# Optimization experiments

Measured on AMD Instinct MI355X. Metric: run time of the kernel, lower is better.

## Reference

```python
import jax, jax.numpy as jnp
import numpy as np

N = 768          # number of proposals (graph nodes)
C = 1024         # box_head feature dim (in_feats)
HC = 256         # RelPN hidden_c
K = 20           # topk edges per node
GH = 256         # gcn_hidden
H1 = 4           # gat1 heads
IMG_H, IMG_W = 800.0, 800.0
NEG_SLOPE = 0.2  # PyG GATConv leaky_relu slope


def setup_inputs() -> dict:
    key = jax.random.key(0)
    ks = jax.random.split(key, 24)
    s = 0.02
    feats = jax.random.normal(ks[0], (N, C), jnp.float32)
    # valid boxes inside an 800x800 image
    cx = jax.random.uniform(ks[1], (N,), minval=100.0, maxval=700.0)
    cy = jax.random.uniform(ks[2], (N,), minval=100.0, maxval=700.0)
    w = jax.random.uniform(ks[3], (N,), minval=10.0, maxval=200.0)
    h = jax.random.uniform(ks[4], (N,), minval=10.0, maxval=200.0)
    boxes = jnp.stack([cx - 0.5 * w, cy - 0.5 * h, cx + 0.5 * w, cy + 0.5 * h], axis=1)
    rn = lambda k, sh: jax.random.normal(k, sh, jnp.float32) * s
    return {
        'feats': feats, 'boxes': boxes,
        # RelationProposalNetwork: fc1(2C+4 -> HC), fc2(HC -> 1)
        'W1': rn(ks[5], (2 * C + 4, HC)), 'b1': jnp.zeros((HC,), jnp.float32),
        'W2': rn(ks[6], (HC, 1)), 'b2': jnp.zeros((1,), jnp.float32),
        # GATConv(C+4 -> GH, heads=4)
        'g1W': rn(ks[7], (C + 4, H1 * GH)), 'g1as': rn(ks[8], (H1, GH)),
        'g1ad': rn(ks[9], (H1, GH)), 'g1b': jnp.zeros((H1 * GH,), jnp.float32),
        # GATConv(GH*4 -> 2, heads=1)
        'g2W': rn(ks[10], (H1 * GH, 2)), 'g2as': rn(ks[11], (1, 2)),
        'g2ad': rn(ks[12], (1, 2)), 'g2b': jnp.zeros((2,), jnp.float32),
        'rW1': rn(ks[13], (H1 * GH + 4, GH // 2)), 'rb1': jnp.zeros((GH // 2,), jnp.float32),
        'rW2': rn(ks[14], (GH // 2, 4)), 'rb2': jnp.zeros((4,), jnp.float32),
    }


def _gat(xin, W, a_src, a_dst, bias, heads, feat, nbr):
    """PyG-style GATConv (eval mode, self-loops already in nbr). nbr: [N, K+1] src ids per dst."""
    n = xin.shape[0]
    xp = (xin @ W).reshape(n, heads, feat)              # [N,H,F]
    asrc = jnp.einsum('nhf,hf->nh', xp, a_src)          # [N,H]
    adst = jnp.einsum('nhf,hf->nh', xp, a_dst)          # [N,H]
    logits = jax.nn.leaky_relu(asrc[nbr] + adst[:, None, :], NEG_SLOPE)  # [N,K+1,H]
    alpha = jax.nn.softmax(logits, axis=1)              # softmax over incoming edges per dst
    out = jnp.einsum('nkh,nkhf->nhf', alpha, xp[nbr])   # gather + weighted aggregate
    return out.reshape(n, heads * feat) + bias


def reference(feats, boxes, W1, b1, W2, b2, g1W, g1as, g1ad, g1b,
              g2W, g2as, g2ad, g2b, rW1, rb1, rW2, rb2):
    n = feats.shape[0]
    scale = jnp.array([IMG_W, IMG_H, IMG_W, IMG_H], jnp.float32)
    geom = boxes / scale                                 # _box_geom: normalized coords
    x = jnp.concatenate([feats, geom], axis=1)           # [N, C+4]

    # --- RelationProposalNetwork: fc1(cat[f_i, f_j, |b_i - b_j|]) decomposed ---
    Wa, Wb, Wg = W1[:C], W1[C:2 * C], W1[2 * C:]
    fa = feats @ Wa                                      # i-part  [N,HC]
    fb = feats @ Wb                                      # j-part  [N,HC]
    gdiff = jnp.abs(boxes[:, None, :] - boxes[None, :, :])          # [N,N,4]
    h = jax.nn.relu(fa[:, None, :] + fb[None, :, :]
                    + jnp.einsum('ijd,dh->ijh', gdiff, Wg) + b1)    # [N,N,HC]
    rel = jnp.einsum('ijh,h->ij', h, W2[:, 0]) + b2[0]              # [N,N]

    # --- top-k edges per destination node (exclude self), plus self-loops ---
    rel_masked = jnp.where(jnp.eye(n, dtype=bool), -1e9, rel)
    _, nbr = jax.lax.top_k(rel_masked, K)                # [N,K] src j for each dst i
    nbr = jnp.concatenate([nbr, jnp.arange(n)[:, None]], axis=1)    # [N,K+1]

    # --- GAT propagation ---
    h1 = jax.nn.relu(_gat(x, g1W, g1as, g1ad, g1b, H1, GH, nbr))    # [N,1024]
    logits = _gat(h1, g2W, g2as, g2ad, g2b, 1, 2, nbr)              # [N,2]

    reg_in = jnp.concatenate([h1, geom], axis=1)
    delta = jax.nn.relu(reg_in @ rW1 + rb1) @ rW2 + rb2             # [N,4]
    px0, py0, px1, py1 = boxes[:, 0], boxes[:, 1], boxes[:, 2], boxes[:, 3]
    pw, ph = px1 - px0, py1 - py0
    pcx, pcy = px0 + 0.5 * pw, py0 + 0.5 * ph
    dx, dy, dw, dh = delta[:, 0], delta[:, 1], delta[:, 2], delta[:, 3]
    gcx, gcy = dx * pw + pcx, dy * ph + pcy
    gw, gh = jnp.exp(dw) * pw, jnp.exp(dh) * ph
    final_boxes = jnp.stack([gcx - 0.5 * gw, gcy - 0.5 * gh,
                             gcx + 0.5 * gw, gcy + 0.5 * gh], axis=1)
    return jnp.concatenate([logits, final_boxes], axis=1)  # [N,6]
```

## Files before the change

### kernel.cpp

```cpp
#include <hip/hip_runtime.h>
#include <math.h>

#define NN 768
#define KK_TOP 20
#define NBR_K 21

typedef __attribute__((ext_vector_type(8))) short bf16x8;
typedef __attribute__((ext_vector_type(4))) float f32x4;
typedef unsigned short ushort_t;
typedef unsigned int uint_t;

__device__ __forceinline__ ushort_t f2bf(float x) {
    union { float f; uint_t u; } c; c.f = x;
    uint_t r = (c.u + 0x7FFFu + ((c.u >> 16) & 1u)) >> 16;
    return (ushort_t)r;
}
__device__ __forceinline__ float bf2f(ushort_t u) {
    union { uint_t u; float f; } c; c.u = ((uint_t)u) << 16;
    return c.f;
}

struct Params {
    const float *feats, *boxes, *W1, *b1, *W2, *b2;
    const float *g1W, *g1as, *g1ad, *g1b, *g2W, *g2as, *g2ad, *g2b;
    const float *rW1, *rb1, *rW2, *rb2;
    float *out;
    float *fafb, *xp, *relm, *hid, *Arow, *Brow, *asrc, *adst, *xp2, *aux2;
    float4 *wgt4; float *w2p, *consts;
    float *va, *vb, *av;
    int *nbr;
    ushort_t *featsbf, *btAB, *btG, *btR, *h1bf;
};

__global__ __launch_bounds__(256) void k_prep(Params P)
{
    int b = blockIdx.x, t = threadIdx.x;
    if (b == 800) {
        const float* Wg = P.W1 + 2048 * 256;
        float q0 = Wg[t], q1 = Wg[256 + t], q2 = Wg[512 + t], q3 = Wg[768 + t];
        float w2 = P.W2[t];
        P.wgt4[t] = make_float4(q0, q1, q2, q3);
        P.w2p[t] = w2;
        __shared__ float red[256];
        float vals[5] = {q0 * w2, q1 * w2, q2 * w2, q3 * w2, P.b1[t] * w2};
        for (int d = 0; d < 5; d++) {
            red[t] = vals[d]; __syncthreads();
            for (int s = 128; s > 0; s >>= 1) {
                if (t < s) red[t] += red[t + s];
                __syncthreads();
            }
            if (t == 0) P.consts[d] = red[0];
            __syncthreads();
        }
        return;
    }
    if (b >= 1313) {
        int o = (b - 1313) * 4 + (t >> 6);
        int lane = t & 63;
        if (o >= 8224) return;
        int vec = o / 1028, k = o - vec * 1028;
        int h = vec & 3;
        const float4* aw = (const float4*)(((vec < 4) ? P.g1as : P.g1ad) + h * 256);
        const float4* gw = (const float4*)(P.g1W + (size_t)k * 1024 + h * 256);
        float4 a = aw[lane], g = gw[lane];
        float s = a.x * g.x + a.y * g.y + a.z * g.z + a.w * g.w;
#pragma unroll
        for (int off = 32; off > 0; off >>= 1) s += __shfl_xor(s, off);
        if (lane == 0) P.av[o] = s;
        return;
    }
    if (b >= 801) {
        int o = (b - 801) * 4 + (t >> 6);
        int lane = t & 63;
        const float4* row = (const float4*)(P.W1 + (size_t)o * 256);
        float4 w = ((const float4*)P.W2)[lane];
        float4 f = row[lane];
        float s = f.x * w.x + f.y * w.y + f.z * w.z + f.w * w.w;
#pragma unroll
        for (int off = 32; off > 0; off >>= 1) s += __shfl_xor(s, off);
        if (lane == 0) { if (o < 1024) P.va[o] = s; else P.vb[o - 1024] = s; }
        return;
    }
    if (b >= 416) {
        int gid = (b - 416) * 2048 + t * 8;
        float4 v0 = *(const float4*)(P.feats + gid);
        float4 v1 = *(const float4*)(P.feats + gid + 4);
        uint4 r;
        r.x = (uint_t)f2bf(v0.x) | ((uint_t)f2bf(v0.y) << 16);
        r.y = (uint_t)f2bf(v0.z) | ((uint_t)f2bf(v0.w) << 16);
        r.z = (uint_t)f2bf(v1.x) | ((uint_t)f2bf(v1.y) << 16);
        r.w = (uint_t)f2bf(v1.z) | ((uint_t)f2bf(v1.w) << 16);
        *(uint4*)(P.featsbf + gid) = r;
        return;
    }
    const float* in; ushort_t* out; int ldN, tk, tn;
    if (b < 64)       { in = P.W1;              out = P.btAB;              ldN = 256;  tn = b & 3;  tk = b >> 2; }
    else if (b < 128) { int i = b - 64;  in = P.W1 + 1024 * 256; out = P.btAB + 256 * 1024; ldN = 256;  tn = i & 3;  tk = i >> 2; }
    else if (b < 384) { int i = b - 128; in = P.g1W;             out = P.btG;               ldN = 1024; tn = i & 15; tk = i >> 4; }
    else              { int i = b - 384; in = P.rW1;             out = P.btR;               ldN = 128;  tn = i & 1;  tk = i >> 1; }

    __shared__ __align__(16) float tile[64][68];
    int k0 = tk * 64, n0 = tn * 64;
#pragma unroll
    for (int it = 0; it < 4; it++) {
        int r = (t >> 4) + it * 16;
        int c = (t & 15) * 4;
        *(float4*)&tile[r][c] = *(const float4*)(in + (size_t)(k0 + r) * ldN + n0 + c);
    }
    __syncthreads();
    int n = t >> 2;
    int kc = (t & 3) * 16;
    uint_t p[8];
#pragma unroll
    for (int h = 0; h < 8; h++) {
        ushort_t lo = f2bf(tile[kc + 2 * h][n]);
        ushort_t hi = f2bf(tile[kc + 2 * h + 1][n]);
        p[h] = (uint_t)lo | ((uint_t)hi << 16);
    }
    ushort_t* dst = out + (size_t)(n0 + n) * 1024 + k0 + kc;
    *(uint4*)dst = make_uint4(p[0], p[1], p[2], p[3]);
    *(uint4*)(dst + 8) = make_uint4(p[4], p[5], p[6], p[7]);
}

__device__ __forceinline__ void mfma_unit(
    int bx, int by, const ushort_t* __restrict__ A, const ushort_t* __restrict__ Bt,
    float* __restrict__ C, int ldc, int mode,
    const float* __restrict__ boxes, const float* __restrict__ Wgeo,
    const float* __restrict__ bias, int t, char* smem)
{
    ushort_t (*As)[72] = (ushort_t(*)[72])smem;
    ushort_t (*Bs)[72] = (ushort_t(*)[72])(smem + 64 * 72 * 2);
    int m0 = by * 64, n0 = bx * 64;
    int lane = t & 63, w = t >> 6;
    int quad = lane >> 4, ci = lane & 15;

    int r0 = t >> 3, q0 = t & 7;
    int r1 = (t + 256) >> 3, q1 = (t + 256) & 7;

    const ushort_t* Abase = A + (size_t)(m0 + r0) * 1024 + q0 * 8;
    const ushort_t* Abase1 = A + (size_t)(m0 + r1) * 1024 + q1 * 8;
    const ushort_t* Bbase = Bt + (size_t)(n0 + r0) * 1024 + q0 * 8;
    const ushort_t* Bbase1 = Bt + (size_t)(n0 + r1) * 1024 + q1 * 8;

    uint4 pa0 = *(const uint4*)(Abase);
    uint4 pa1 = *(const uint4*)(Abase1);
    uint4 pb0 = *(const uint4*)(Bbase);
    uint4 pb1 = *(const uint4*)(Bbase1);

    f32x4 acc[2][2];
    acc[0][0] = (f32x4){0.f, 0.f, 0.f, 0.f};
    acc[0][1] = (f32x4){0.f, 0.f, 0.f, 0.f};
    acc[1][0] = (f32x4){0.f, 0.f, 0.f, 0.f};
    acc[1][1] = (f32x4){0.f, 0.f, 0.f, 0.f};

    int arow = (w & 1) * 32 + ci;
    int brow = (w >> 1) * 32 + ci;

    for (int kt = 0; kt < 16; kt++) {
        *(uint4*)&As[r0][q0 * 8] = pa0;
        *(uint4*)&As[r1][q1 * 8] = pa1;
        *(uint4*)&Bs[r0][q0 * 8] = pb0;
        *(uint4*)&Bs[r1][q1 * 8] = pb1;
        __syncthreads();
        if (kt < 15) {
            int ko = (kt + 1) * 64;
            pa0 = *(const uint4*)(Abase + ko);
            pa1 = *(const uint4*)(Abase1 + ko);
            pb0 = *(const uint4*)(Bbase + ko);
            pb1 = *(const uint4*)(Bbase1 + ko);
        }
#pragma unroll
        for (int s = 0; s < 2; s++) {
            int kb = s * 32 + quad * 8;
            bf16x8 a0 = *(const bf16x8*)&As[arow][kb];
            bf16x8 a1 = *(const bf16x8*)&As[arow + 16][kb];
            bf16x8 b0 = *(const bf16x8*)&Bs[brow][kb];
            bf16x8 b1 = *(const bf16x8*)&Bs[brow + 16][kb];
            acc[0][0] = __builtin_amdgcn_mfma_f32_16x16x32_bf16(a0, b0, acc[0][0], 0, 0, 0);
            acc[0][1] = __builtin_amdgcn_mfma_f32_16x16x32_bf16(a0, b1, acc[0][1], 0, 0, 0);
            acc[1][0] = __builtin_amdgcn_mfma_f32_16x16x32_bf16(a1, b0, acc[1][0], 0, 0, 0);
            acc[1][1] = __builtin_amdgcn_mfma_f32_16x16x32_bf16(a1, b1, acc[1][1], 0, 0, 0);
        }
        __syncthreads();
    }

    const float inv800 = 1.0f / 800.0f;
#pragma unroll
    for (int ni = 0; ni < 2; ni++) {
        int col = n0 + (w >> 1) * 32 + ni * 16 + ci;
        float wg0 = 0.f, wg1 = 0.f, wg2 = 0.f, wg3 = 0.f, bv = 0.f;
        if (mode) {
            wg0 = Wgeo[col]; wg1 = Wgeo[ldc + col];
            wg2 = Wgeo[2 * ldc + col]; wg3 = Wgeo[3 * ldc + col];
            if (mode == 2) bv = bias[col];
        }
#pragma unroll
        for (int mi = 0; mi < 2; mi++) {
            int rbase = m0 + (w & 1) * 32 + mi * 16 + quad * 4;
#pragma unroll
            for (int reg = 0; reg < 4; reg++) {
                int row = rbase + reg;
                float v = acc[mi][ni][reg];
                if (mode) {
                    float4 bx4 = *(const float4*)(boxes + row * 4);
                    v += (bx4.x * wg0 + bx4.y * wg1 + bx4.z * wg2 + bx4.w * wg3) * inv800 + bv;
                    if (mode == 2) v = fmaxf(v, 0.f);
                }
                C[(size_t)row * ldc + col] = v;
            }
        }
    }
}

__global__ __launch_bounds__(256) void k_gemms(Params P)
{
    __shared__ __align__(16) char smem[18432];
    int u = blockIdx.x, t = threadIdx.x;
    if (u < 96) {
        mfma_unit(u & 7, u >> 3, P.featsbf, P.btAB, P.fafb, 512, 0,
                  nullptr, nullptr, nullptr, t, smem);
    } else if (u < 288) {
        int v = u - 96;
        mfma_unit(v & 15, v >> 4, P.featsbf, P.btG, P.xp, 1024, 1,
                  P.boxes, P.g1W + (size_t)1024 * 1024, nullptr, t, smem);
    } else if (u < 480) {
        int row = (u - 288) * 4 + (t >> 6);
        int lane = t & 63;
        const float4* fr = (const float4*)(P.feats + (size_t)row * 1024);
        const float4* va4 = (const float4*)P.va;
        const float4* vb4 = (const float4*)P.vb;
        float s1 = 0.f, s2 = 0.f;
#pragma unroll
        for (int it = 0; it < 4; it++) {
            int idx = it * 64 + lane;
            float4 f = fr[idx], a = va4[idx], b = vb4[idx];
            s1 += f.x * a.x + f.y * a.y + f.z * a.z + f.w * a.w;
            s2 += f.x * b.x + f.y * b.y + f.z * b.z + f.w * b.w;
        }
#pragma unroll
        for (int off = 32; off > 0; off >>= 1) {
            s1 += __shfl_xor(s1, off);
            s2 += __shfl_xor(s2, off);
        }
        if (lane == 0) { P.Arow[row] = s1; P.Brow[row] = s2; }
    } else {
        int pair = (u - 480) * 4 + (t >> 6);
        int lane = t & 63;
        int n = pair >> 2, h = pair & 3;
        const float4* fr = (const float4*)(P.feats + (size_t)n * 1024);
        const float* vs = P.av + h * 1028;
        const float* vd = P.av + (4 + h) * 1028;
        const float4* vs4 = (const float4*)vs;
        const float4* vd4 = (const float4*)vd;
        float s1 = 0.f, s2 = 0.f;
#pragma unroll
        for (int it = 0; it < 4; it++) {
            int idx = it * 64 + lane;
            float4 f = fr[idx], a = vs4[idx], b = vd4[idx];
            s1 += f.x * a.x + f.y * a.y + f.z * a.z + f.w * a.w;
            s2 += f.x * b.x + f.y * b.y + f.z * b.z + f.w * b.w;
        }
#pragma unroll
        for (int off = 32; off > 0; off >>= 1) {
            s1 += __shfl_xor(s1, off);
            s2 += __shfl_xor(s2, off);
        }
        if (lane == 0) {
            const float inv800 = 1.0f / 800.0f;
            float4 bx = *(const float4*)(P.boxes + n * 4);
            float g0 = bx.x * inv800, g1 = bx.y * inv800, g2 = bx.z * inv800, g3 = bx.w * inv800;
            s1 += g0 * vs[1024] + g1 * vs[1025] + g2 * vs[1026] + g3 * vs[1027];
            s2 += g0 * vd[1024] + g1 * vd[1025] + g2 * vd[1026] + g3 * vd[1027];
            P.asrc[n * 4 + h] = s1;
            P.adst[n * 4 + h] = s2;
        }
    }
}

#define REL_ACC(FA0, FA1, FB0, FB1, Q, W)                                           \
    {                                                                               \
        float v;                                                                    \
        v = FA0 + FB0;                                                              \
        v = fmaf(g00.x, Q.x, v); v = fmaf(g00.y, Q.y, v);                           \
        v = fmaf(g00.z, Q.z, v); v = fmaf(g00.w, Q.w, v);                           \
        acc00 = fmaf(fabsf(v), W, acc00);                                           \
        v = FA0 + FB1;                                                              \
        v = fmaf(g01.x, Q.x, v); v = fmaf(g01.y, Q.y, v);                           \
        v = fmaf(g01.z, Q.z, v); v = fmaf(g01.w, Q.w, v);                           \
        acc01 = fmaf(fabsf(v), W, acc01);                                           \
        v = FA1 + FB0;                                                              \
        v = fmaf(g10.x, Q.x, v); v = fmaf(g10.y, Q.y, v);                           \
        v = fmaf(g10.z, Q.z, v); v = fmaf(g10.w, Q.w, v);                           \
        acc10 = fmaf(fabsf(v), W, acc10);                                           \
        v = FA1 + FB1;                                                              \
        v = fmaf(g11.x, Q.x, v); v = fmaf(g11.y, Q.y, v);                           \
        v = fmaf(g11.z, Q.z, v); v = fmaf(g11.w, Q.w, v);                           \
        acc11 = fmaf(fabsf(v), W, acc11);                                           \
    }

__global__ __launch_bounds__(256) void k_rel(Params P)
{
    __shared__ __align__(16) float fas[32][68];
    __shared__ __align__(16) float fbs[32][68];
    int t = threadIdx.x;
    int bx = blockIdx.x % 24, by = blockIdx.x / 24;
    int tx = t & 15, ty = t >> 4;
    int i0 = by * 32, j0 = bx * 32;
    int ia = i0 + ty, ib = i0 + ty + 16;
    int ja = j0 + tx, jb = j0 + tx + 16;

    float4 Bi0 = *(const float4*)(P.boxes + ia * 4);
    float4 Bi1 = *(const float4*)(P.boxes + ib * 4);
    float4 Bj0 = *(const float4*)(P.boxes + ja * 4);
    float4 Bj1 = *(const float4*)(P.boxes + jb * 4);
    float4 g00 = make_float4(fabsf(Bi0.x - Bj0.x), fabsf(Bi0.y - Bj0.y), fabsf(Bi0.z - Bj0.z), fabsf(Bi0.w - Bj0.w));
    float4 g01 = make_float4(fabsf(Bi0.x - Bj1.x), fabsf(Bi0.y - Bj1.y), fabsf(Bi0.z - Bj1.z), fabsf(Bi0.w - Bj1.w));
    float4 g10 = make_float4(fabsf(Bi1.x - Bj0.x), fabsf(Bi1.y - Bj0.y), fabsf(Bi1.z - Bj0.z), fabsf(Bi1.w - Bj0.w));
    float4 g11 = make_float4(fabsf(Bi1.x - Bj1.x), fabsf(Bi1.y - Bj1.y), fabsf(Bi1.z - Bj1.z), fabsf(Bi1.w - Bj1.w));

    float acc00 = 0.f, acc01 = 0.f, acc10 = 0.f, acc11 = 0.f;

    for (int p = 0; p < 4; p++) {
        for (int e = t; e < 512; e += 256) {
            int r = e >> 4, cq = e & 15;
            float4 bb = *(const float4*)(P.b1 + p * 64 + cq * 4);
            float4 fv = *(const float4*)(P.fafb + (size_t)(i0 + r) * 512 + p * 64 + cq * 4);
            float4 gv = *(const float4*)(P.fafb + (size_t)(j0 + r) * 512 + 256 + p * 64 + cq * 4);
            *(float4*)&fas[r][cq * 4] = make_float4(fv.x + bb.x, fv.y + bb.y, fv.z + bb.z, fv.w + bb.w);
            *(float4*)&fbs[r][cq * 4] = gv;
        }
        __syncthreads();
        const float4* wg = P.wgt4 + p * 64;
        const float* w2 = P.w2p + p * 64;
#pragma unroll 8
        for (int hc = 0; hc < 16; hc++) {
            int h4 = hc * 4;
            float4 fa0 = *(const float4*)&fas[ty][h4];
            float4 fa1 = *(const float4*)&fas[ty + 16][h4];
            float4 fb0 = *(const float4*)&fbs[tx][h4];
            float4 fb1 = *(const float4*)&fbs[tx + 16][h4];
            float4 w2v = *(const float4*)(w2 + h4);
            float4 q0 = wg[h4], q1 = wg[h4 + 1], q2 = wg[h4 + 2], q3 = wg[h4 + 3];
            REL_ACC(fa0.x, fa1.x, fb0.x, fb1.x, q0, w2v.x);
            REL_ACC(fa0.y, fa1.y, fb0.y, fb1.y, q1, w2v.y);
            REL_ACC(fa0.z, fa1.z, fb0.z, fb1.z, q2, w2v.z);
            REL_ACC(fa0.w, fa1.w, fb0.w, fb1.w, q3, w2v.w);
        }
        __syncthreads();
    }

    float c0 = P.consts[0], c1 = P.consts[1], c2 = P.consts[2], c3 = P.consts[3], c4 = P.consts[4];
    float b2v = P.b2[0];
    float Ai0 = P.Arow[ia], Ai1 = P.Arow[ib];
    float Bja = P.Brow[ja], Bjb = P.Brow[jb];

    float lin, r00, r01, r10, r11;
    lin = Ai0 + Bja + g00.x * c0 + g00.y * c1 + g00.z * c2 + g00.w * c3 + c4;
    r00 = 0.5f * (lin + acc00) + b2v;
    lin = Ai0 + Bjb + g01.x * c0 + g01.y * c1 + g01.z * c2 + g01.w * c3 + c4;
    r01 = 0.5f * (lin + acc01) + b2v;
    lin = Ai1 + Bja + g10.x * c0 + g10.y * c1 + g10.z * c2 + g10.w * c3 + c4;
    r10 = 0.5f * (lin + acc10) + b2v;
    lin = Ai1 + Bjb + g11.x * c0 + g11.y * c1 + g11.z * c2 + g11.w * c3 + c4;
    r11 = 0.5f * (lin + acc11) + b2v;
    P.relm[(size_t)ia * NN + ja] = (ia == ja) ? -1e9f : r00;
    P.relm[(size_t)ia * NN + jb] = (ia == jb) ? -1e9f : r01;
    P.relm[(size_t)ib * NN + ja] = (ib == ja) ? -1e9f : r10;
    P.relm[(size_t)ib * NN + jb] = (ib == jb) ? -1e9f : r11;
}

__global__ __launch_bounds__(256) void k_topkgat1(Params P)
{
    int n = blockIdx.x, t = threadIdx.x;
    __shared__ int nb[NBR_K];
    __shared__ float alpha[NBR_K][4];

    if (t < 64) {
        int lane = t;
        const float* rp = P.relm + (size_t)n * NN;
        float v[12];
#pragma unroll
        for (int q = 0; q < 12; q++) v[q] = rp[q * 64 + lane];
        for (int kk = 0; kk < KK_TOP; kk++) {
            float best = v[0]; int bq = 0;
#pragma unroll
            for (int q = 1; q < 12; q++) {
                if (v[q] > best) { best = v[q]; bq = q; }
            }
            int bidx = bq * 64 + lane;
#pragma unroll
            for (int off = 32; off > 0; off >>= 1) {
                float ov = __shfl_xor(best, off);
                int oi = __shfl_xor(bidx, off);
                if (ov > best || (ov == best && oi < bidx)) { best = ov; bidx = oi; }
            }
            if (lane == 0) { nb[kk] = bidx; P.nbr[n * NBR_K + kk] = bidx; }
            int bl = bidx & 63, bq2 = bidx >> 6;
            if (lane == bl) {
#pragma unroll
                for (int q = 0; q < 12; q++)
                    if (q == bq2) v[q] = -INFINITY;
            }
        }
        if (lane == 0) { nb[KK_TOP] = n; P.nbr[n * NBR_K + KK_TOP] = n; }
    }
    __syncthreads();

    if (t < NBR_K * 4) {
        int k = t % NBR_K, h = t / NBR_K;
        float e = P.asrc[nb[k] * 4 + h] + P.adst[n * 4 + h];
        e = (e > 0.f) ? e : 0.2f * e;
        alpha[k][h] = e;
    }
    __syncthreads();
    if (t < 4) {
        float m = -INFINITY;
        for (int k = 0; k < NBR_K; k++) m = fmaxf(m, alpha[k][t]);
        float s = 0.f;
        for (int k = 0; k < NBR_K; k++) { float ex = expf(alpha[k][t] - m); alpha[k][t] = ex; s += ex; }
        float inv = 1.f / s;
        for (int k = 0; k < NBR_K; k++) alpha[k][t] *= inv;
    }
    __syncthreads();

    int h = t >> 6;
    float ax = 0.f, ay = 0.f, az = 0.f, aw = 0.f;
#pragma unroll 7
    for (int k = 0; k < NBR_K; k++) {
        float a = alpha[k][h];
        float4 xv = ((const float4*)(P.xp + (size_t)nb[k] * 1024))[t];
        ax = fmaf(a, xv.x, ax); ay = fmaf(a, xv.y, ay);
        az = fmaf(a, xv.z, az); aw = fmaf(a, xv.w, aw);
    }
    float4 gb = ((const float4*)P.g1b)[t];
    uint2 pk;
    pk.x = (uint_t)f2bf(fmaxf(ax + gb.x, 0.f)) | ((uint_t)f2bf(fmaxf(ay + gb.y, 0.f)) << 16);
    pk.y = (uint_t)f2bf(fmaxf(az + gb.z, 0.f)) | ((uint_t)f2bf(fmaxf(aw + gb.w, 0.f)) << 16);
    *(uint2*)(P.h1bf + (size_t)n * 1024 + t * 4) = pk;
}

__global__ __launch_bounds__(256) void k_p6(Params P)
{
    __shared__ __align__(16) char smem[18432];
    int u = blockIdx.x, t = threadIdx.x;
    if (u < 192) {
        int wid = u * 4 + (t >> 6);
        int lane = t & 63;
        float s0 = 0.f, s1 = 0.f;
#pragma unroll
        for (int it = 0; it < 4; it++) {
            int k = it * 256 + lane * 4;
            uint2 pk = *(const uint2*)(P.h1bf + (size_t)wid * 1024 + k);
            float v0 = bf2f((ushort_t)(pk.x & 0xFFFF));
            float v1 = bf2f((ushort_t)(pk.x >> 16));
            float v2 = bf2f((ushort_t)(pk.y & 0xFFFF));
            float v3 = bf2f((ushort_t)(pk.y >> 16));
            float4 w0 = *(const float4*)(P.g2W + k * 2);
            float4 w1 = *(const float4*)(P.g2W + k * 2 + 4);
            s0 += v0 * w0.x + v1 * w0.z + v2 * w1.x + v3 * w1.z;
            s1 += v0 * w0.y + v1 * w0.w + v2 * w1.y + v3 * w1.w;
        }
#pragma unroll
        for (int off = 32; off > 0; off >>= 1) { s0 += __shfl_down(s0, off); s1 += __shfl_down(s1, off); }
        if (lane == 0) {
            P.xp2[wid * 2 + 0] = s0; P.xp2[wid * 2 + 1] = s1;
            P.aux2[wid * 2 + 0] = s0 * P.g2as[0] + s1 * P.g2as[1];
            P.aux2[wid * 2 + 1] = s0 * P.g2ad[0] + s1 * P.g2ad[1];
        }
    } else {
        int v = u - 192;
        mfma_unit(v & 1, v >> 1, P.h1bf, P.btR, P.hid, 128, 2,
                  P.boxes, P.rW1 + (size_t)1024 * 128, P.rb1, t, smem);
    }
}

__global__ __launch_bounds__(256) void k_p7(Params P)
{
    __shared__ __align__(16) float rw2s[512];
    int u = blockIdx.x, t = threadIdx.x;
    if (u < 192) {
        int n = u * 4 + (t >> 6);
        int lane = t & 63;
        float adstv = P.aux2[n * 2 + 1];
        float e = -INFINITY, x0 = 0.f, x1 = 0.f;
        if (lane < NBR_K) {
            int nbk = P.nbr[n * NBR_K + lane];
            float vv = P.aux2[nbk * 2 + 0] + adstv;
            e = (vv > 0.f) ? vv : 0.2f * vv;
            x0 = P.xp2[nbk * 2 + 0];
            x1 = P.xp2[nbk * 2 + 1];
        }
        float m = e;
#pragma unroll
        for (int off = 32; off > 0; off >>= 1) m = fmaxf(m, __shfl_xor(m, off));
        float ex = (lane < NBR_K) ? expf(e - m) : 0.f;
        float ssum = ex, o0 = ex * x0, o1 = ex * x1;
#pragma unroll
        for (int off = 32; off > 0; off >>= 1) {
            ssum += __shfl_xor(ssum, off);
            o0 += __shfl_xor(o0, off);
            o1 += __shfl_xor(o1, off);
        }
        if (lane == 0) {
            float inv = 1.f / ssum;
            P.out[n * 6 + 0] = o0 * inv + P.g2b[0];
            P.out[n * 6 + 1] = o1 * inv + P.g2b[1];
        }
        return;
    }
    *(float2*)&rw2s[t * 2] = *(const float2*)(P.rW2 + t * 2);
    __syncthreads();
    int n = (u - 192) * 256 + t;
    const float4* hrow = (const float4*)(P.hid + (size_t)n * 128);
    float d0 = 0.f, d1 = 0.f, d2 = 0.f, d3 = 0.f;
#pragma unroll 8
    for (int k4 = 0; k4 < 32; k4++) {
        float4 h = hrow[k4];
        const float* wv = &rw2s[k4 * 16];
        d0 = fmaf(h.x, wv[0], d0);  d1 = fmaf(h.x, wv[1], d1);
        d2 = fmaf(h.x, wv[2], d2);  d3 = fmaf(h.x, wv[3], d3);
        d0 = fmaf(h.y, wv[4], d0);  d1 = fmaf(h.y, wv[5], d1);
        d2 = fmaf(h.y, wv[6], d2);  d3 = fmaf(h.y, wv[7], d3);
        d0 = fmaf(h.z, wv[8], d0);  d1 = fmaf(h.z, wv[9], d1);
        d2 = fmaf(h.z, wv[10], d2); d3 = fmaf(h.z, wv[11], d3);
        d0 = fmaf(h.w, wv[12], d0); d1 = fmaf(h.w, wv[13], d1);
        d2 = fmaf(h.w, wv[14], d2); d3 = fmaf(h.w, wv[15], d3);
    }
    d0 += P.rb2[0]; d1 += P.rb2[1]; d2 += P.rb2[2]; d3 += P.rb2[3];
    float4 bx = *(const float4*)(P.boxes + n * 4);
    float pw = bx.z - bx.x, ph = bx.w - bx.y;
    float pcx = bx.x + 0.5f * pw, pcy = bx.y + 0.5f * ph;
    float gcx = d0 * pw + pcx, gcy = d1 * ph + pcy;
    float gw = expf(d2) * pw, gh = expf(d3) * ph;
    P.out[n * 6 + 2] = gcx - 0.5f * gw;
    P.out[n * 6 + 3] = gcy - 0.5f * gh;
    P.out[n * 6 + 4] = gcx + 0.5f * gw;
    P.out[n * 6 + 5] = gcy + 0.5f * gh;
}

extern "C" void kernel_launch(void* const* d_in, const int* in_sizes, int n_in,
                              void* d_out, int out_size, void* d_ws, size_t ws_size,
                              hipStream_t stream)
{
    Params P;
    P.feats = (const float*)d_in[0];
    P.boxes = (const float*)d_in[1];
    P.W1    = (const float*)d_in[2];
    P.b1    = (const float*)d_in[3];
    P.W2    = (const float*)d_in[4];
    P.b2    = (const float*)d_in[5];
    P.g1W   = (const float*)d_in[6];
    P.g1as  = (const float*)d_in[7];
    P.g1ad  = (const float*)d_in[8];
    P.g1b   = (const float*)d_in[9];
    P.g2W   = (const float*)d_in[10];
    P.g2as  = (const float*)d_in[11];
    P.g2ad  = (const float*)d_in[12];
    P.g2b   = (const float*)d_in[13];
    P.rW1   = (const float*)d_in[14];
    P.rb1   = (const float*)d_in[15];
    P.rW2   = (const float*)d_in[16];
    P.rb2   = (const float*)d_in[17];
    P.out   = (float*)d_out;

    float* ws = (float*)d_ws;
    P.fafb  = ws;
    P.xp    = P.fafb + 393216;
    P.relm  = P.xp + 786432;
    P.hid   = P.relm + 589824;
    P.Arow  = P.hid + 98304;
    P.Brow  = P.Arow + 768;
    P.asrc  = P.Brow + 768;
    P.adst  = P.asrc + 3072;
    P.xp2   = P.adst + 3072;
    P.aux2  = P.xp2 + 1536;
    P.wgt4  = (float4*)(P.aux2 + 1536);
    P.w2p   = (float*)(P.wgt4 + 256);
    P.consts= P.w2p + 256;
    P.va    = P.consts + 8;
    P.vb    = P.va + 1024;
    P.av    = P.vb + 1024;
    P.nbr   = (int*)(P.av + 8224);
    P.featsbf = (ushort_t*)(P.nbr + 16128);
    P.btAB    = P.featsbf + 786432;
    P.btG     = P.btAB + 524288;
    P.btR     = P.btG + 1048576;
    P.h1bf    = P.btR + 131072;

    k_prep    <<<dim3(3369), dim3(256), 0, stream>>>(P);
    k_gemms   <<<dim3(1248), dim3(256), 0, stream>>>(P);
    k_rel     <<<dim3(576),  dim3(256), 0, stream>>>(P);
    k_topkgat1<<<dim3(768),  dim3(256), 0, stream>>>(P);
    k_p6      <<<dim3(216),  dim3(256), 0, stream>>>(P);
    k_p7      <<<dim3(195),  dim3(256), 0, stream>>>(P);
}
```

Measured before the change: 184.1 us.

## Derive linear relation terms and GAT attention scores from existing GEMM outputs

The separate fp32 passes are removed: one projected W1 through W2 into va/vb, another projected g1W through the attention vectors, and both then dotted every feats row. Instead, k_rel accumulates the linear relation term from the fa/fb tiles it already loads, using four extra FMAs per step. Extra k_rel blocks now compute asrc/adst directly from the xp GEMM output. This cuts thousands of blocks and repeated full reads of feats from k_prep and k_gemms. In exchange it adds arithmetic to the rel inner loop, and it relies on fafb already including the b1 bias, since the separate c4 constant is dropped.

```diff
diff --git a/kernel.cpp b/kernel.cpp
--- a/kernel.cpp
+++ b/kernel.cpp
@@ -25,9 +25,8 @@
     const float *g1W, *g1as, *g1ad, *g1b, *g2W, *g2as, *g2ad, *g2b;
     const float *rW1, *rb1, *rW2, *rb2;
     float *out;
-    float *fafb, *xp, *relm, *hid, *Arow, *Brow, *asrc, *adst, *xp2, *aux2;
+    float *fafb, *xp, *relm, *hid, *asrc, *adst, *xp2, *aux2;
     float4 *wgt4; float *w2p, *consts;
-    float *va, *vb, *av;
     int *nbr;
     ushort_t *featsbf, *btAB, *btG, *btR, *h1bf;
 };
@@ -42,8 +41,8 @@
         P.wgt4[t] = make_float4(q0, q1, q2, q3);
         P.w2p[t] = w2;
         __shared__ float red[256];
-        float vals[5] = {q0 * w2, q1 * w2, q2 * w2, q3 * w2, P.b1[t] * w2};
-        for (int d = 0; d < 5; d++) {
+        float vals[4] = {q0 * w2, q1 * w2, q2 * w2, q3 * w2};
+        for (int d = 0; d < 4; d++) {
             red[t] = vals[d]; __syncthreads();
             for (int s = 128; s > 0; s >>= 1) {
                 if (t < s) red[t] += red[t + s];
@@ -52,33 +51,6 @@
             if (t == 0) P.consts[d] = red[0];
             __syncthreads();
         }
-        return;
-    }
-    if (b >= 1313) {
-        int o = (b - 1313) * 4 + (t >> 6);
-        int lane = t & 63;
-        if (o >= 8224) return;
-        int vec = o / 1028, k = o - vec * 1028;
-        int h = vec & 3;
-        const float4* aw = (const float4*)(((vec < 4) ? P.g1as : P.g1ad) + h * 256);
-        const float4* gw = (const float4*)(P.g1W + (size_t)k * 1024 + h * 256);
-        float4 a = aw[lane], g = gw[lane];
-        float s = a.x * g.x + a.y * g.y + a.z * g.z + a.w * g.w;
-#pragma unroll
-        for (int off = 32; off > 0; off >>= 1) s += __shfl_xor(s, off);
-        if (lane == 0) P.av[o] = s;
-        return;
-    }
-    if (b >= 801) {
-        int o = (b - 801) * 4 + (t >> 6);
-        int lane = t & 63;
-        const float4* row = (const float4*)(P.W1 + (size_t)o * 256);
-        float4 w = ((const float4*)P.W2)[lane];
-        float4 f = row[lane];
-        float s = f.x * w.x + f.y * w.y + f.z * w.z + f.w * w.w;
-#pragma unroll
-        for (int off = 32; off > 0; off >>= 1) s += __shfl_xor(s, off);
-        if (lane == 0) { if (o < 1024) P.va[o] = s; else P.vb[o - 1024] = s; }
         return;
     }
     if (b >= 416) {
@@ -219,61 +191,10 @@
     if (u < 96) {
         mfma_unit(u & 7, u >> 3, P.featsbf, P.btAB, P.fafb, 512, 0,
                   nullptr, nullptr, nullptr, t, smem);
-    } else if (u < 288) {
+    } else {
         int v = u - 96;
         mfma_unit(v & 15, v >> 4, P.featsbf, P.btG, P.xp, 1024, 1,
                   P.boxes, P.g1W + (size_t)1024 * 1024, nullptr, t, smem);
-    } else if (u < 480) {
-        int row = (u - 288) * 4 + (t >> 6);
-        int lane = t & 63;
-        const float4* fr = (const float4*)(P.feats + (size_t)row * 1024);
-        const float4* va4 = (const float4*)P.va;
-        const float4* vb4 = (const float4*)P.vb;
-        float s1 = 0.f, s2 = 0.f;
-#pragma unroll
-        for (int it = 0; it < 4; it++) {
-            int idx = it * 64 + lane;
-            float4 f = fr[idx], a = va4[idx], b = vb4[idx];
-            s1 += f.x * a.x + f.y * a.y + f.z * a.z + f.w * a.w;
-            s2 += f.x * b.x + f.y * b.y + f.z * b.z + f.w * b.w;
-        }
-#pragma unroll
-        for (int off = 32; off > 0; off >>= 1) {
-            s1 += __shfl_xor(s1, off);
-            s2 += __shfl_xor(s2, off);
-        }
-        if (lane == 0) { P.Arow[row] = s1; P.Brow[row] = s2; }
-    } else {
-        int pair = (u - 480) * 4 + (t >> 6);
-        int lane = t & 63;
-        int n = pair >> 2, h = pair & 3;
-        const float4* fr = (const float4*)(P.feats + (size_t)n * 1024);
-        const float* vs = P.av + h * 1028;
-        const float* vd = P.av + (4 + h) * 1028;
-        const float4* vs4 = (const float4*)vs;
-        const float4* vd4 = (const float4*)vd;
-        float s1 = 0.f, s2 = 0.f;
-#pragma unroll
-        for (int it = 0; it < 4; it++) {
-            int idx = it * 64 + lane;
-            float4 f = fr[idx], a = vs4[idx], b = vd4[idx];
-            s1 += f.x * a.x + f.y * a.y + f.z * a.z + f.w * a.w;
-            s2 += f.x * b.x + f.y * b.y + f.z * b.z + f.w * b.w;
-        }
-#pragma unroll
-        for (int off = 32; off > 0; off >>= 1) {
-            s1 += __shfl_xor(s1, off);
-            s2 += __shfl_xor(s2, off);
-        }
-        if (lane == 0) {
-            const float inv800 = 1.0f / 800.0f;
-            float4 bx = *(const float4*)(P.boxes + n * 4);
-            float g0 = bx.x * inv800, g1 = bx.y * inv800, g2 = bx.z * inv800, g3 = bx.w * inv800;
-            s1 += g0 * vs[1024] + g1 * vs[1025] + g2 * vs[1026] + g3 * vs[1027];
-            s2 += g0 * vd[1024] + g1 * vd[1025] + g2 * vd[1026] + g3 * vd[1027];
-            P.asrc[n * 4 + h] = s1;
-            P.adst[n * 4 + h] = s2;
-        }
     }
 }
 
@@ -296,14 +217,36 @@
         v = fmaf(g11.x, Q.x, v); v = fmaf(g11.y, Q.y, v);                           \
         v = fmaf(g11.z, Q.z, v); v = fmaf(g11.w, Q.w, v);                           \
         acc11 = fmaf(fabsf(v), W, acc11);                                           \
+        sA0 = fmaf(FA0, W, sA0); sA1 = fmaf(FA1, W, sA1);                           \
+        sB0 = fmaf(FB0, W, sB0); sB1 = fmaf(FB1, W, sB1);                           \
     }
 
 __global__ __launch_bounds__(256) void k_rel(Params P)
 {
+    int t = threadIdx.x;
+    int u = blockIdx.x;
+    if (u >= 576) {
+        int wv = (u - 576) * 4 + (t >> 6);
+        int lane = t & 63;
+        int n = wv >> 2, h = wv & 3;
+        const float4* xr = (const float4*)(P.xp + (size_t)n * 1024 + h * 256);
+        const float4* wsrc = (const float4*)(P.g1as + h * 256);
+        const float4* wdst = (const float4*)(P.g1ad + h * 256);
+        float4 x4 = xr[lane], a4 = wsrc[lane], b4 = wdst[lane];
+        float s1 = x4.x * a4.x + x4.y * a4.y + x4.z * a4.z + x4.w * a4.w;
+        float s2 = x4.x * b4.x + x4.y * b4.y + x4.z * b4.z + x4.w * b4.w;
+#pragma unroll
+        for (int off = 32; off > 0; off >>= 1) {
+            s1 += __shfl_xor(s1, off);
+            s2 += __shfl_xor(s2, off);
+        }
+        if (lane == 0) { P.asrc[wv] = s1; P.adst[wv] = s2; }
+        return;
+    }
+
     __shared__ __align__(16) float fas[32][68];
     __shared__ __align__(16) float fbs[32][68];
-    int t = threadIdx.x;
-    int bx = blockIdx.x % 24, by = blockIdx.x / 24;
+    int bx = u % 24, by = u / 24;
     int tx = t & 15, ty = t >> 4;
     int i0 = by * 32, j0 = bx * 32;
     int ia = i0 + ty, ib = i0 + ty + 16;
@@ -319,6 +262,7 @@
     float4 g11 = make_float4(fabsf(Bi1.x - Bj1.x), fabsf(Bi1.y - Bj1.y), fabsf(Bi1.z - Bj1.z), fabsf(Bi1.w - Bj1.w));
 
     float acc00 = 0.f, acc01 = 0.f, acc10 = 0.f, acc11 = 0.f;
+    float sA0 = 0.f, sA1 = 0.f, sB0 = 0.f, sB1 = 0.f;
 
     for (int p = 0; p < 4; p++) {
         for (int e = t; e < 512; e += 256) {
@@ -349,19 +293,17 @@
         __syncthreads();
     }
 
-    float c0 = P.consts[0], c1 = P.consts[1], c2 = P.consts[2], c3 = P.consts[3], c4 = P.consts[4];
+    float c0 = P.consts[0], c1 = P.consts[1], c2 = P.consts[2], c3 = P.consts[3];
     float b2v = P.b2[0];
-    float Ai0 = P.Arow[ia], Ai1 = P.Arow[ib];
-    float Bja = P.Brow[ja], Bjb = P.Brow[jb];
 
     float lin, r00, r01, r10, r11;
-    lin = Ai0 + Bja + g00.x * c0 + g00.y * c1 + g00.z * c2 + g00.w * c3 + c4;
+    lin = sA0 + sB0 + g00.x * c0 + g00.y * c1 + g00.z * c2 + g00.w * c3;
     r00 = 0.5f * (lin + acc00) + b2v;
-    lin = Ai0 + Bjb + g01.x * c0 + g01.y * c1 + g01.z * c2 + g01.w * c3 + c4;
+    lin = sA0 + sB1 + g01.x * c0 + g01.y * c1 + g01.z * c2 + g01.w * c3;
     r01 = 0.5f * (lin + acc01) + b2v;
-    lin = Ai1 + Bja + g10.x * c0 + g10.y * c1 + g10.z * c2 + g10.w * c3 + c4;
+    lin = sA1 + sB0 + g10.x * c0 + g10.y * c1 + g10.z * c2 + g10.w * c3;
     r10 = 0.5f * (lin + acc10) + b2v;
-    lin = Ai1 + Bjb + g11.x * c0 + g11.y * c1 + g11.z * c2 + g11.w * c3 + c4;
+    lin = sA1 + sB1 + g11.x * c0 + g11.y * c1 + g11.z * c2 + g11.w * c3;
     r11 = 0.5f * (lin + acc11) + b2v;
     P.relm[(size_t)ia * NN + ja] = (ia == ja) ? -1e9f : r00;
     P.relm[(size_t)ia * NN + jb] = (ia == jb) ? -1e9f : r01;
@@ -568,28 +510,23 @@
     P.xp    = P.fafb + 393216;
     P.relm  = P.xp + 786432;
     P.hid   = P.relm + 589824;
-    P.Arow  = P.hid + 98304;
-    P.Brow  = P.Arow + 768;
-    P.asrc  = P.Brow + 768;
+    P.asrc  = P.hid + 98304;
     P.adst  = P.asrc + 3072;
     P.xp2   = P.adst + 3072;
     P.aux2  = P.xp2 + 1536;
     P.wgt4  = (float4*)(P.aux2 + 1536);
     P.w2p   = (float*)(P.wgt4 + 256);
     P.consts= P.w2p + 256;
-    P.va    = P.consts + 8;
-    P.vb    = P.va + 1024;
-    P.av    = P.vb + 1024;
-    P.nbr   = (int*)(P.av + 8224);
+    P.nbr   = (int*)(P.consts + 8);
     P.featsbf = (ushort_t*)(P.nbr + 16128);
     P.btAB    = P.featsbf + 786432;
     P.btG     = P.btAB + 524288;
     P.btR     = P.btG + 1048576;
     P.h1bf    = P.btR + 131072;
 
-    k_prep    <<<dim3(3369), dim3(256), 0, stream>>>(P);
-    k_gemms   <<<dim3(1248), dim3(256), 0, stream>>>(P);
-    k_rel     <<<dim3(576),  dim3(256), 0, stream>>>(P);
+    k_prep    <<<dim3(801),  dim3(256), 0, stream>>>(P);
+    k_gemms   <<<dim3(288),  dim3(256), 0, stream>>>(P);
+    k_rel     <<<dim3(1344), dim3(256), 0, stream>>>(P);
     k_topkgat1<<<dim3(768),  dim3(256), 0, stream>>>(P);
     k_p6      <<<dim3(216),  dim3(256), 0, stream>>>(P);
     k_p7      <<<dim3(195),  dim3(256), 0, stream>>>(P);
```

Result: slower. 188.0 us (+2.1%).

## Split k_rel hidden-dim reduction across two block halves to double parallelism

Applied to the files above, without the earlier changes.

The relation-score kernel now launches twice as many blocks, with each half reducing over half of the 256 hidden channels and writing a partial score matrix. The top-k kernel sums the two partial matrices when it loads each row. This targets low occupancy from only 576 blocks on a GPU with many CUs, at the cost of an extra 768x768 buffer written and read back. The diagonal is -1e9 in the first half and 0 in the second, so masking still holds after the sum.

```diff
diff --git a/kernel.cpp b/kernel.cpp
--- a/kernel.cpp
+++ b/kernel.cpp
@@ -303,7 +303,10 @@
     __shared__ __align__(16) float fas[32][68];
     __shared__ __align__(16) float fbs[32][68];
     int t = threadIdx.x;
-    int bx = blockIdx.x % 24, by = blockIdx.x / 24;
+    int u = blockIdx.x;
+    int half = (u >= 576) ? 1 : 0;
+    int ub = u - half * 576;
+    int bx = ub % 24, by = ub / 24;
     int tx = t & 15, ty = t >> 4;
     int i0 = by * 32, j0 = bx * 32;
     int ia = i0 + ty, ib = i0 + ty + 16;
@@ -320,7 +323,8 @@
 
     float acc00 = 0.f, acc01 = 0.f, acc10 = 0.f, acc11 = 0.f;
 
-    for (int p = 0; p < 4; p++) {
+    for (int pp = 0; pp < 2; pp++) {
+        int p = half * 2 + pp;
         for (int e = t; e < 512; e += 256) {
             int r = e >> 4, cq = e & 15;
             float4 bb = *(const float4*)(P.b1 + p * 64 + cq * 4);
@@ -349,24 +353,31 @@
         __syncthreads();
     }
 
-    float c0 = P.consts[0], c1 = P.consts[1], c2 = P.consts[2], c3 = P.consts[3], c4 = P.consts[4];
-    float b2v = P.b2[0];
-    float Ai0 = P.Arow[ia], Ai1 = P.Arow[ib];
-    float Bja = P.Brow[ja], Bjb = P.Brow[jb];
-
-    float lin, r00, r01, r10, r11;
-    lin = Ai0 + Bja + g00.x * c0 + g00.y * c1 + g00.z * c2 + g00.w * c3 + c4;
-    r00 = 0.5f * (lin + acc00) + b2v;
-    lin = Ai0 + Bjb + g01.x * c0 + g01.y * c1 + g01.z * c2 + g01.w * c3 + c4;
-    r01 = 0.5f * (lin + acc01) + b2v;
-    lin = Ai1 + Bja + g10.x * c0 + g10.y * c1 + g10.z * c2 + g10.w * c3 + c4;
-    r10 = 0.5f * (lin + acc10) + b2v;
-    lin = Ai1 + Bjb + g11.x * c0 + g11.y * c1 + g11.z * c2 + g11.w * c3 + c4;
-    r11 = 0.5f * (lin + acc11) + b2v;
-    P.relm[(size_t)ia * NN + ja] = (ia == ja) ? -1e9f : r00;
-    P.relm[(size_t)ia * NN + jb] = (ia == jb) ? -1e9f : r01;
-    P.relm[(size_t)ib * NN + ja] = (ib == ja) ? -1e9f : r10;
-    P.relm[(size_t)ib * NN + jb] = (ib == jb) ? -1e9f : r11;
+    float* relh = P.relm + (size_t)half * NN * NN;
+    if (half == 0) {
+        float c0 = P.consts[0], c1 = P.consts[1], c2 = P.consts[2], c3 = P.consts[3], c4 = P.consts[4];
+        float b2v = P.b2[0];
+        float Ai0 = P.Arow[ia], Ai1 = P.Arow[ib];
+        float Bja = P.Brow[ja], Bjb = P.Brow[jb];
+        float lin, r00, r01, r10, r11;
+        lin = Ai0 + Bja + g00.x * c0 + g00.y * c1 + g00.z * c2 + g00.w * c3 + c4;
+        r00 = 0.5f * (lin + acc00) + b2v;
+        lin = Ai0 + Bjb + g01.x * c0 + g01.y * c1 + g01.z * c2 + g01.w * c3 + c4;
+        r01 = 0.5f * (lin + acc01) + b2v;
+        lin = Ai1 + Bja + g10.x * c0 + g10.y * c1 + g10.z * c2 + g10.w * c3 + c4;
+        r10 = 0.5f * (lin + acc10) + b2v;
+        lin = Ai1 + Bjb + g11.x * c0 + g11.y * c1 + g11.z * c2 + g11.w * c3 + c4;
+        r11 = 0.5f * (lin + acc11) + b2v;
+        relh[(size_t)ia * NN + ja] = (ia == ja) ? -1e9f : r00;
+        relh[(size_t)ia * NN + jb] = (ia == jb) ? -1e9f : r01;
+        relh[(size_t)ib * NN + ja] = (ib == ja) ? -1e9f : r10;
+        relh[(size_t)ib * NN + jb] = (ib == jb) ? -1e9f : r11;
+    } else {
+        relh[(size_t)ia * NN + ja] = (ia == ja) ? 0.f : 0.5f * acc00;
+        relh[(size_t)ia * NN + jb] = (ia == jb) ? 0.f : 0.5f * acc01;
+        relh[(size_t)ib * NN + ja] = (ib == ja) ? 0.f : 0.5f * acc10;
+        relh[(size_t)ib * NN + jb] = (ib == jb) ? 0.f : 0.5f * acc11;
+    }
 }
 
 __global__ __launch_bounds__(256) void k_topkgat1(Params P)
@@ -377,10 +388,11 @@
 
     if (t < 64) {
         int lane = t;
-        const float* rp = P.relm + (size_t)n * NN;
+        const float* rp0 = P.relm + (size_t)n * NN;
+        const float* rp1 = P.relm + (size_t)NN * NN + (size_t)n * NN;
         float v[12];
 #pragma unroll
-        for (int q = 0; q < 12; q++) v[q] = rp[q * 64 + lane];
+        for (int q = 0; q < 12; q++) v[q] = rp0[q * 64 + lane] + rp1[q * 64 + lane];
         for (int kk = 0; kk < KK_TOP; kk++) {
             float best = v[0]; int bq = 0;
 #pragma unroll
@@ -567,7 +579,7 @@
     P.fafb  = ws;
     P.xp    = P.fafb + 393216;
     P.relm  = P.xp + 786432;
-    P.hid   = P.relm + 589824;
+    P.hid   = P.relm + 2 * 589824;
     P.Arow  = P.hid + 98304;
     P.Brow  = P.Arow + 768;
     P.asrc  = P.Brow + 768;
@@ -589,7 +601,7 @@
 
     k_prep    <<<dim3(3369), dim3(256), 0, stream>>>(P);
     k_gemms   <<<dim3(1248), dim3(256), 0, stream>>>(P);
-    k_rel     <<<dim3(576),  dim3(256), 0, stream>>>(P);
+    k_rel     <<<dim3(1152), dim3(256), 0, stream>>>(P);
     k_topkgat1<<<dim3(768),  dim3(256), 0, stream>>>(P);
     k_p6      <<<dim3(216),  dim3(256), 0, stream>>>(P);
     k_p7      <<<dim3(195),  dim3(256), 0, stream>>>(P);
```

Measured after the change: 176.8 us. -4.0%, faster.
